# Optimization experiments

Hardware: AMD Instinct MI355X
Metric: run time of the kernel (lower is better)

The kernel has to match this reference:

```python
import jax, jax.numpy as jnp
import numpy as np

B, IN_DIM, UNITS = 2048, 256, 512

def setup_inputs() -> dict:
    key = jax.random.key(0)
    k1, k2 = jax.random.split(key)
    x = jax.random.uniform(k1, (B, IN_DIM), dtype=jnp.float32)
    weights = jax.random.uniform(k2, (IN_DIM * UNITS,), dtype=jnp.float32)
    return {"x": x, "weights": weights}

def reference(x, weights):
    # kernel: [in_dim, units]; transpose -> [units, in_dim]
    in_dim = x.shape[-1]
    kT = weights.reshape(in_dim, UNITS).T  # [units, in_dim]
    # broadcast multiply-add: [B, 1, in_dim] * [units, in_dim] + (1 - kT)
    # -> [B, units, in_dim]; product-reduce over in_dim (XOR via bipolar product)
    t = x[:, None, :] * kT + (1.0 - kT)
    return jnp.prod(t, axis=-1)  # [B, units]
```

## Files before the change

### kernel.cpp

```cpp
#include <hip/hip_runtime.h>


#define B_DIM    2048
#define IN_DIM   256
#define UNITS    512
#define TB       8
#define BLOCK    256

__global__ __launch_bounds__(BLOCK) void prodw_kernel(
    const float* __restrict__ x,
    const float* __restrict__ w,
    float* __restrict__ out)
{
    const int u  = blockIdx.x * BLOCK + threadIdx.x;
    const int b0 = blockIdx.y * TB;

    const float* __restrict__ xrow = x + (size_t)b0 * IN_DIM;

    float p[TB];
#pragma unroll
    for (int j = 0; j < TB; ++j) p[j] = 1.0f;

#pragma unroll 4
    for (int i = 0; i < IN_DIM; ++i) {
        const float wv = w[(size_t)i * UNITS + u];
        const float c  = 1.0f - wv;
#pragma unroll
        for (int j = 0; j < TB; ++j) {
            const float xv = xrow[j * IN_DIM + i];
            p[j] *= fmaf(xv, wv, c);
        }
    }

#pragma unroll
    for (int j = 0; j < TB; ++j)
        out[(size_t)(b0 + j) * UNITS + u] = p[j];
}

extern "C" void kernel_launch(void* const* d_in, const int* in_sizes, int n_in,
                              void* d_out, int out_size, void* d_ws, size_t ws_size,
                              hipStream_t stream) {
    const float* x = (const float*)d_in[0];
    const float* w = (const float*)d_in[1];
    float* out     = (float*)d_out;

    dim3 grid(UNITS / BLOCK, B_DIM / TB);
    dim3 block(BLOCK);
    prodw_kernel<<<grid, block, 0, stream>>>(x, w, out);
}
```

Baseline: 81.50 us.

## Stage x tile in shared memory and software-prefetch weights in groups of four

Each block loads its 8 rows of x into LDS using float4 loads. The inner loop then reads x as float4 from LDS instead of issuing scalar global loads. Weights are loaded four rows ahead in registers as a software prefetch. The multiply chain is reassociated as a tree ((t0*t1)*(t2*t3)) to shorten the dependency chain. This targets redundant global/L1 traffic and load latency, at the cost of LDS use, a barrier, and floating-point reassociation that can change rounding.

```diff
diff --git a/kernel.cpp b/kernel.cpp
--- a/kernel.cpp
+++ b/kernel.cpp
@@ -7,28 +7,74 @@
 #define TB       8
 #define BLOCK    256
 
-__global__ __launch_bounds__(BLOCK) void prodw_kernel(
+__global__ __launch_bounds__(BLOCK, 2) void prodw_kernel(
     const float* __restrict__ x,
     const float* __restrict__ w,
     float* __restrict__ out)
 {
-    const int u  = blockIdx.x * BLOCK + threadIdx.x;
-    const int b0 = blockIdx.y * TB;
+    __shared__ __align__(16) float xs[TB * IN_DIM];
 
-    const float* __restrict__ xrow = x + (size_t)b0 * IN_DIM;
+    const int tid = threadIdx.x;
+    const int u   = blockIdx.x * BLOCK + tid;
+    const int b0  = blockIdx.y * TB;
+
+    {
+        const float4* __restrict__ xg = (const float4*)(x + (size_t)b0 * IN_DIM);
+        float4* xl = (float4*)xs;
+        xl[tid]         = xg[tid];
+        xl[tid + BLOCK] = xg[tid + BLOCK];
+    }
+    __syncthreads();
 
     float p[TB];
 #pragma unroll
     for (int j = 0; j < TB; ++j) p[j] = 1.0f;
 
-#pragma unroll 4
-    for (int i = 0; i < IN_DIM; ++i) {
-        const float wv = w[(size_t)i * UNITS + u];
-        const float c  = 1.0f - wv;
+    const float* __restrict__ wu = w + u;
+
+    float w0 = wu[0 * UNITS];
+    float w1 = wu[1 * UNITS];
+    float w2 = wu[2 * UNITS];
+    float w3 = wu[3 * UNITS];
+
+    for (int g = 0; g < (IN_DIM / 4) - 1; ++g) {
+        const int i4 = g * 4;
+        const float* __restrict__ wn = wu + (size_t)(i4 + 4) * UNITS;
+        const float n0 = wn[0 * UNITS];
+        const float n1 = wn[1 * UNITS];
+        const float n2 = wn[2 * UNITS];
+        const float n3 = wn[3 * UNITS];
+
+        const float c0 = 1.0f - w0;
+        const float c1 = 1.0f - w1;
+        const float c2 = 1.0f - w2;
+        const float c3 = 1.0f - w3;
 #pragma unroll
         for (int j = 0; j < TB; ++j) {
-            const float xv = xrow[j * IN_DIM + i];
-            p[j] *= fmaf(xv, wv, c);
+            const float4 xq = *(const float4*)&xs[j * IN_DIM + i4];
+            const float t0 = fmaf(xq.x, w0, c0);
+            const float t1 = fmaf(xq.y, w1, c1);
+            const float t2 = fmaf(xq.z, w2, c2);
+            const float t3 = fmaf(xq.w, w3, c3);
+            p[j] *= (t0 * t1) * (t2 * t3);
+        }
+        w0 = n0; w1 = n1; w2 = n2; w3 = n3;
+    }
+
+    {
+        const int i4 = IN_DIM - 4;
+        const float c0 = 1.0f - w0;
+        const float c1 = 1.0f - w1;
+        const float c2 = 1.0f - w2;
+        const float c3 = 1.0f - w3;
+#pragma unroll
+        for (int j = 0; j < TB; ++j) {
+            const float4 xq = *(const float4*)&xs[j * IN_DIM + i4];
+            const float t0 = fmaf(xq.x, w0, c0);
+            const float t1 = fmaf(xq.y, w1, c1);
+            const float t2 = fmaf(xq.z, w2, c2);
+            const float t3 = fmaf(xq.w, w3, c3);
+            p[j] *= (t0 * t1) * (t2 * t3);
         }
     }
 
```

After: 77.16 us. 1.06x faster.

## Use packed float2 FMA/mul with software-prefetched float4 x loads

Applied to the files above, without the earlier changes.

Rewrites the inner loop to process four input dims per step using packed two-wide float vectors (v_pk_fma_f32 / v_pk_mul_f32), splitting each product into two partial accumulators that are combined at the end. x rows are loaded as float4 and the next group's weights and x values are prefetched one iteration ahead to overlap loads with compute. This aims to halve VALU instruction count and hide load latency, at the cost of more registers and a changed multiplication order, which can alter rounding.

```diff
diff --git a/kernel.cpp b/kernel.cpp
--- a/kernel.cpp
+++ b/kernel.cpp
@@ -1,5 +1,7 @@
 #include <hip/hip_runtime.h>
 
+
+typedef float v2f __attribute__((ext_vector_type(2)));
 
 #define B_DIM    2048
 #define IN_DIM   256
@@ -16,25 +18,70 @@
     const int b0 = blockIdx.y * TB;
 
     const float* __restrict__ xrow = x + (size_t)b0 * IN_DIM;
+    const float* __restrict__ wu   = w + u;
 
-    float p[TB];
+    v2f pp[TB];
 #pragma unroll
-    for (int j = 0; j < TB; ++j) p[j] = 1.0f;
+    for (int j = 0; j < TB; ++j) pp[j] = (v2f){1.0f, 1.0f};
 
-#pragma unroll 4
-    for (int i = 0; i < IN_DIM; ++i) {
-        const float wv = w[(size_t)i * UNITS + u];
-        const float c  = 1.0f - wv;
+    float w0 = wu[0 * UNITS];
+    float w1 = wu[1 * UNITS];
+    float w2 = wu[2 * UNITS];
+    float w3 = wu[3 * UNITS];
+    float4 xq[TB];
+#pragma unroll
+    for (int j = 0; j < TB; ++j)
+        xq[j] = *(const float4*)(xrow + j * IN_DIM);
+
+    for (int g = 0; g < IN_DIM / 4 - 1; ++g) {
+        const int i4 = g * 4;
+
+        const float* __restrict__ wn = wu + (size_t)(i4 + 4) * UNITS;
+        const float n0 = wn[0 * UNITS];
+        const float n1 = wn[1 * UNITS];
+        const float n2 = wn[2 * UNITS];
+        const float n3 = wn[3 * UNITS];
+        float4 xn[TB];
+#pragma unroll
+        for (int j = 0; j < TB; ++j)
+            xn[j] = *(const float4*)(xrow + j * IN_DIM + i4 + 4);
+
+        const v2f wv01 = {w0, w1};
+        const v2f wv23 = {w2, w3};
+        const v2f c01  = (v2f){1.0f, 1.0f} - wv01;
+        const v2f c23  = (v2f){1.0f, 1.0f} - wv23;
 #pragma unroll
         for (int j = 0; j < TB; ++j) {
-            const float xv = xrow[j * IN_DIM + i];
-            p[j] *= fmaf(xv, wv, c);
+            const v2f x01 = {xq[j].x, xq[j].y};
+            const v2f x23 = {xq[j].z, xq[j].w};
+            const v2f t01 = __builtin_elementwise_fma(x01, wv01, c01);
+            const v2f t23 = __builtin_elementwise_fma(x23, wv23, c23);
+            pp[j] *= t01 * t23;
+        }
+
+        w0 = n0; w1 = n1; w2 = n2; w3 = n3;
+#pragma unroll
+        for (int j = 0; j < TB; ++j) xq[j] = xn[j];
+    }
+
+    {
+        const v2f wv01 = {w0, w1};
+        const v2f wv23 = {w2, w3};
+        const v2f c01  = (v2f){1.0f, 1.0f} - wv01;
+        const v2f c23  = (v2f){1.0f, 1.0f} - wv23;
+#pragma unroll
+        for (int j = 0; j < TB; ++j) {
+            const v2f x01 = {xq[j].x, xq[j].y};
+            const v2f x23 = {xq[j].z, xq[j].w};
+            const v2f t01 = __builtin_elementwise_fma(x01, wv01, c01);
+            const v2f t23 = __builtin_elementwise_fma(x23, wv23, c23);
+            pp[j] *= t01 * t23;
         }
     }
 
 #pragma unroll
     for (int j = 0; j < TB; ++j)
-        out[(size_t)(b0 + j) * UNITS + u] = p[j];
+        out[(size_t)(b0 + j) * UNITS + u] = pp[j].x * pp[j].y;
 }
 
 extern "C" void kernel_launch(void* const* d_in, const int* in_sizes, int n_in,
```

New measurement: 75.88 us. 1.07x faster.

## Tile product-reduce into shared-memory 64x64 blocks with 4x4 register tiles

Applied to the files above, without the earlier changes.

Replaces the per-thread column loop, which read x through broadcast global loads, with a shared-memory tiled scheme. Each 256-thread block stages 64x64 chunks of x (transposed) and w in LDS and computes a 4x4 register tile of outputs per thread using float4 LDS reads. This cuts global and cache traffic and raises arithmetic intensity per load, at the cost of LDS usage, two barriers per chunk, and possible bank conflicts on the transposed x stores.

```diff
diff --git a/kernel.cpp b/kernel.cpp
--- a/kernel.cpp
+++ b/kernel.cpp
@@ -1,40 +1,88 @@
 #include <hip/hip_runtime.h>
 
 
-#define B_DIM    2048
-#define IN_DIM   256
-#define UNITS    512
-#define TB       8
-#define BLOCK    256
+#define B_DIM   2048
+#define IN_DIM  256
+#define UNITS   512
+#define BT      64
+#define UT      64
+#define KI      64
+#define BLOCK   256
 
 __global__ __launch_bounds__(BLOCK) void prodw_kernel(
     const float* __restrict__ x,
     const float* __restrict__ w,
     float* __restrict__ out)
 {
-    const int u  = blockIdx.x * BLOCK + threadIdx.x;
-    const int b0 = blockIdx.y * TB;
+    __shared__ __align__(16) float xs[KI][BT];
+    __shared__ __align__(16) float ws[KI][UT];
 
-    const float* __restrict__ xrow = x + (size_t)b0 * IN_DIM;
+    const int tid  = threadIdx.x;
+    const int tx   = tid & 15;
+    const int ty   = tid >> 4;
+    const int ublk = blockIdx.x * UT;
+    const int bblk = blockIdx.y * BT;
 
-    float p[TB];
+    float acc[4][4];
 #pragma unroll
-    for (int j = 0; j < TB; ++j) p[j] = 1.0f;
+    for (int a = 0; a < 4; ++a)
+#pragma unroll
+        for (int b = 0; b < 4; ++b) acc[a][b] = 1.0f;
 
-#pragma unroll 4
-    for (int i = 0; i < IN_DIM; ++i) {
-        const float wv = w[(size_t)i * UNITS + u];
-        const float c  = 1.0f - wv;
+    const int bl   = tid & 63;
+    const int half = tid >> 6;
+
+    for (int ic = 0; ic < IN_DIM / KI; ++ic) {
+        const int ibase = ic * KI;
+
+        {
+            const float* __restrict__ xr =
+                x + (size_t)(bblk + bl) * IN_DIM + ibase + half * 16;
 #pragma unroll
-        for (int j = 0; j < TB; ++j) {
-            const float xv = xrow[j * IN_DIM + i];
-            p[j] *= fmaf(xv, wv, c);
+            for (int r = 0; r < 4; ++r) {
+                const float4 f = *(const float4*)(xr + r * 4);
+                const int i0 = half * 16 + r * 4;
+                xs[i0 + 0][bl] = f.x;
+                xs[i0 + 1][bl] = f.y;
+                xs[i0 + 2][bl] = f.z;
+                xs[i0 + 3][bl] = f.w;
+            }
         }
+        {
+#pragma unroll
+            for (int r = 0; r < 4; ++r) {
+                const int idx = r * BLOCK + tid;
+                const int il  = idx >> 4;
+                const int u4  = (idx & 15) * 4;
+                const float4 f = *(const float4*)
+                    (w + (size_t)(ibase + il) * UNITS + ublk + u4);
+                *(float4*)&ws[il][u4] = f;
+            }
+        }
+        __syncthreads();
+
+#pragma unroll 8
+        for (int il = 0; il < KI; ++il) {
+            const float4 xq = *(const float4*)&xs[il][ty * 4];
+            const float4 wq = *(const float4*)&ws[il][tx * 4];
+            const float xv[4] = {xq.x, xq.y, xq.z, xq.w};
+            const float wv[4] = {wq.x, wq.y, wq.z, wq.w};
+            const float cv[4] = {1.0f - wq.x, 1.0f - wq.y,
+                                 1.0f - wq.z, 1.0f - wq.w};
+#pragma unroll
+            for (int jb = 0; jb < 4; ++jb)
+#pragma unroll
+                for (int ju = 0; ju < 4; ++ju)
+                    acc[jb][ju] *= fmaf(xv[jb], wv[ju], cv[ju]);
+        }
+        __syncthreads();
     }
 
 #pragma unroll
-    for (int j = 0; j < TB; ++j)
-        out[(size_t)(b0 + j) * UNITS + u] = p[j];
+    for (int jb = 0; jb < 4; ++jb) {
+        const float4 o = {acc[jb][0], acc[jb][1], acc[jb][2], acc[jb][3]};
+        *(float4*)(out + (size_t)(bblk + ty * 4 + jb) * UNITS + ublk + tx * 4) = o;
+    }
 }
 
 extern "C" void kernel_launch(void* const* d_in, const int* in_sizes, int n_in,
@@ -44,7 +92,7 @@
     const float* w = (const float*)d_in[1];
     float* out     = (float*)d_out;
 
-    dim3 grid(UNITS / BLOCK, B_DIM / TB);
+    dim3 grid(UNITS / UT, B_DIM / BT);
     dim3 block(BLOCK);
     prodw_kernel<<<grid, block, 0, stream>>>(x, w, out);
 }
```

Result: slower. 83.67 us (+2.7%).
